# Performance work log

Measured on AMD Instinct MI355X. Metric: run time of the kernel, lower is better.

Reference implementation:

```python
import jax, jax.numpy as jnp
import numpy as np

N_NODES = 50000
N_EDGES = 800000


def _sage_conv(x, src, dst, Wl, Wr, b):
    # PyG SAGEConv (aggr='mean', root_weight=True):
    #   out_i = lin_l(mean_{j->i} x_j) + lin_r(x_i)
    msg = x[src]                                             # [E, F] gather
    agg = jax.ops.segment_sum(msg, dst, num_segments=N_NODES)
    deg = jax.ops.segment_sum(jnp.ones((msg.shape[0],), x.dtype), dst,
                              num_segments=N_NODES)
    agg = agg / jnp.maximum(deg, 1.0)[:, None]               # mean aggregation
    return agg @ Wl + x @ Wr + b


def setup_inputs() -> dict:
    key = jax.random.key(0)
    ks = jax.random.split(key, 9)
    Fin, H1, H2, Fout = 128, 256, 128, 64

    def w(k, fi, fo):
        return jax.random.normal(k, (fi, fo), jnp.float32) / np.sqrt(fi)

    return {
        "x": jax.random.normal(ks[0], (N_NODES, Fin), jnp.float32),
        "edge_index": jax.random.randint(ks[1], (2, N_EDGES), 0, N_NODES,
                                         dtype=jnp.int64),
        "Wl1": w(ks[2], Fin, H1), "Wr1": w(ks[3], Fin, H1),
        "b1": jnp.zeros((H1,), jnp.float32),
        "Wl2": w(ks[4], H1, H2), "Wr2": w(ks[5], H1, H2),
        "b2": jnp.zeros((H2,), jnp.float32),
        "Wl3": w(ks[6], H2, Fout), "Wr3": w(ks[7], H2, Fout),
        "b3": jnp.zeros((Fout,), jnp.float32),
    }


def reference(x, edge_index, Wl1, Wr1, b1, Wl2, Wr2, b2, Wl3, Wr3, b3):
    src, dst = edge_index[0], edge_index[1]
    # conv1 -> ReLU -> (dropout: identity in eval) -> conv2 -> ReLU -> conv3 -> Sigmoid
    h = jax.nn.relu(_sage_conv(x, src, dst, Wl1, Wr1, b1))
    h = jax.nn.relu(_sage_conv(h, src, dst, Wl2, Wr2, b2))
    out = jax.nn.sigmoid(_sage_conv(h, src, dst, Wl3, Wr3, b3))
    return out
```

## Files before the change

kernel.cpp:

```cpp
#include <hip/hip_runtime.h>
#include <cstddef>


using frag  = __attribute__((ext_vector_type(8))) short;
using f32x4 = __attribute__((ext_vector_type(4))) float;
using vf2   = __attribute__((ext_vector_type(2))) float;
typedef unsigned char u8;

constexpr int PBITS = 9;
constexpr int PSZ   = 1 << PBITS;
constexpr int PMAX  = 128;

__device__ __forceinline__ ushort f2bf(float f) {
    union { float f; unsigned u; } v; v.f = f;
    unsigned r = v.u + 0x7FFF + ((v.u >> 16) & 1);
    return (ushort)(r >> 16);
}
__device__ __forceinline__ float bf2f(ushort u) {
    union { unsigned u; float f; } v; v.u = ((unsigned)u) << 16;
    return v.f;
}


__global__ __launch_bounds__(256)
void k_pcount(const int* __restrict__ dst, int* __restrict__ pcount, int E, int P) {
    __shared__ int h[PMAX];
    int t = threadIdx.x;
    if (t < P) h[t] = 0;
    __syncthreads();
    int base = blockIdx.x * 4096;
    int n = min(4096, E - base);
    for (int i = t; i < n; i += 256)
        atomicAdd(&h[dst[base + i] >> PBITS], 1);
    __syncthreads();
    if (t < P && h[t]) atomicAdd(&pcount[t], h[t]);
}

__global__ void k_pscan(const int* __restrict__ pcount, int* __restrict__ pbase,
                        int* __restrict__ pcursor, int P) {
    if (threadIdx.x == 0) {
        int run = 0;
        for (int p = 0; p < P; ++p) { pbase[p] = run; pcursor[p] = run; run += pcount[p]; }
        pbase[P] = run;
    }
}

__global__ __launch_bounds__(256)
void k_scatter(const int* __restrict__ src, const int* __restrict__ dst,
               int* __restrict__ pcursor, unsigned* __restrict__ pairs, int E, int P) {
    __shared__ int h[PMAX];
    __shared__ int off[PMAX];
    int t = threadIdx.x;
    if (t < P) h[t] = 0;
    __syncthreads();
    int base = blockIdx.x * 4096;
    int pp[16]; int pr[16]; unsigned pk[16];
    #pragma unroll
    for (int ii = 0; ii < 16; ++ii) {
        int idx = base + ii * 256 + t;
        bool v = idx < E;
        int d = v ? dst[idx] : 0;
        int p = d >> PBITS;
        pp[ii] = v ? p : -1;
        pr[ii] = v ? atomicAdd(&h[p], 1) : 0;
        pk[ii] = v ? ((unsigned)src[idx] | ((unsigned)(d & (PSZ - 1)) << 16)) : 0u;
    }
    __syncthreads();
    if (t < P && h[t]) off[t] = atomicAdd(&pcursor[t], h[t]);
    __syncthreads();
    #pragma unroll
    for (int ii = 0; ii < 16; ++ii)
        if (pp[ii] >= 0) pairs[off[pp[ii]] + pr[ii]] = pk[ii];
}

__global__ __launch_bounds__(256)
void k_build(const unsigned* __restrict__ pairs, const int* __restrict__ pbase,
             int* __restrict__ deg, int* __restrict__ row_start,
             ushort* __restrict__ csr16, int M) {
    __shared__ int cnt[PSZ];
    __shared__ int ls[PSZ];
    __shared__ int fil[PSZ];
    __shared__ int ws[256];
    int pid = blockIdx.x;
    int t = threadIdx.x;
    int n0 = pid << PBITS;
    int L = min(PSZ, M - n0);
    int wb = pbase[pid], we = pbase[pid + 1];
    int ne = we - wb;
    for (int j = t; j < PSZ; j += 256) { cnt[j] = 0; fil[j] = 0; }
    __syncthreads();
    for (int i = t; i < ne; i += 256)
        atomicAdd(&cnt[pairs[wb + i] >> 16], 1);
    __syncthreads();
    int a = cnt[2 * t], b = cnt[2 * t + 1];
    ws[t] = a + b;
    __syncthreads();
    for (int o = 1; o < 256; o <<= 1) {
        int v = (t >= o) ? ws[t - o] : 0;
        __syncthreads();
        ws[t] += v;
        __syncthreads();
    }
    int excl = (t > 0) ? ws[t - 1] : 0;
    ls[2 * t] = excl; ls[2 * t + 1] = excl + a;
    __syncthreads();
    for (int j = t; j < L; j += 256) {
        deg[n0 + j] = cnt[j];
        row_start[n0 + j] = wb + ls[j];
    }
    for (int i = t; i < ne; i += 256) {
        unsigned pk = pairs[wb + i];
        int ln = pk >> 16;
        int pos = wb + ls[ln] + atomicAdd(&fil[ln], 1);
        csr16[pos] = (ushort)(pk & 0xFFFFu);
    }
}


struct CvtDesc {
    const float* s[6];
    ushort*      d[6];
    int K[6];
    int N[6];
    int KD[6];
    int KO[6];
};

__global__ void k_cvt_all(CvtDesc c, const float* __restrict__ x,
                          ushort* __restrict__ AX, u8* __restrict__ x8,
                          int n4, int xblocks) {
    int bid = blockIdx.x;
    if (bid < xblocks) {
        int i = bid * 256 + threadIdx.x;
        if (i < n4) {
            int row = i >> 5;
            int c4  = i & 31;
            float4 v = ((const float4*)x)[i];
            ushort4 o; o.x = f2bf(v.x); o.y = f2bf(v.y); o.z = f2bf(v.z); o.w = f2bf(v.w);
            *(ushort4*)(AX + (size_t)row * 256 + 128 + c4 * 4) = o;
            int pk = __builtin_amdgcn_cvt_pk_fp8_f32(v.x, v.y, 0, false);
            pk = __builtin_amdgcn_cvt_pk_fp8_f32(v.z, v.w, pk, true);
            *(int*)(x8 + (size_t)row * 128 + c4 * 4) = pk;
        }
    } else {
        int wb = bid - xblocks;
        int wi = wb >> 7;
        int t = (wb & 127) * 256 + threadIdx.x;
        int K = c.K[wi], N = c.N[wi];
        if (t < K * N) {
            int k = t / N, n = t % N;
            c.d[wi][(size_t)n * c.KD[wi] + c.KO[wi] + k] = f2bf(c.s[wi][t]);
        }
    }
}


template <int F, int EPI, int IN8, int LDI, int LDO>
__global__ __launch_bounds__(256)
void agg_bf(const void* __restrict__ inv, const ushort* __restrict__ csr16,
            const int* __restrict__ row_start, const int* __restrict__ deg,
            const ushort* __restrict__ u, const float* __restrict__ bias,
            void* __restrict__ out, int nN) {
    constexpr int GPL = F / 4;
    constexpr int NPB = 256 / GPL;
    int gid  = threadIdx.x / GPL;
    int li   = threadIdx.x % GPL;
    int node = blockIdx.x * NPB + gid;
    bool valid = node < nN;
    int start = valid ? row_start[node] : 0;
    int d     = valid ? deg[node] : 0;
    float a0 = 0.f, a1 = 0.f, a2 = 0.f, a3 = 0.f;

    auto gat = [&](int j) {
        int s = csr16[start + j];
        if constexpr (IN8) {
            int uu = *(const int*)((const u8*)inv + (size_t)s * LDI + li * 4);
            vf2 lo = __builtin_amdgcn_cvt_pk_f32_fp8(uu, false);
            vf2 hi = __builtin_amdgcn_cvt_pk_f32_fp8(uu, true);
            a0 += lo[0]; a1 += lo[1]; a2 += hi[0]; a3 += hi[1];
        } else {
            ushort4 uv = *(const ushort4*)((const ushort*)inv + (size_t)s * LDI + li * 4);
            a0 += bf2f(uv.x); a1 += bf2f(uv.y); a2 += bf2f(uv.z); a3 += bf2f(uv.w);
        }
    };

    int j = 0;
    for (; j + 8 <= d; j += 8) {
        gat(j); gat(j+1); gat(j+2); gat(j+3);
        gat(j+4); gat(j+5); gat(j+6); gat(j+7);
    }
    for (; j + 2 <= d; j += 2) { gat(j); gat(j+1); }
    for (; j < d; ++j) gat(j);

    if (!valid) return;
    float inv_d = 1.f / (float)(d > 0 ? d : 1);
    a0 *= inv_d; a1 *= inv_d; a2 *= inv_d; a3 *= inv_d;

    size_t o4 = (size_t)node * LDO + li * 4;
    if constexpr (EPI == 0) {
        ushort4 o; o.x = f2bf(a0); o.y = f2bf(a1); o.z = f2bf(a2); o.w = f2bf(a3);
        *(ushort4*)((ushort*)out + o4) = o;
    } else {
        ushort4 uv = *(const ushort4*)(u + (size_t)node * F + li * 4);
        float4 bv = *(const float4*)(bias + li * 4);
        a0 += bf2f(uv.x) + bv.x;
        a1 += bf2f(uv.y) + bv.y;
        a2 += bf2f(uv.z) + bv.z;
        a3 += bf2f(uv.w) + bv.w;
        if constexpr (EPI == 1) {
            ushort4 o;
            o.x = f2bf(fmaxf(a0, 0.f)); o.y = f2bf(fmaxf(a1, 0.f));
            o.z = f2bf(fmaxf(a2, 0.f)); o.w = f2bf(fmaxf(a3, 0.f));
            *(ushort4*)((ushort*)out + o4) = o;
        } else {
            float4 o;
            o.x = 1.f / (1.f + __expf(-a0)); o.y = 1.f / (1.f + __expf(-a1));
            o.z = 1.f / (1.f + __expf(-a2)); o.w = 1.f / (1.f + __expf(-a3));
            *(float4*)((float*)out + o4) = o;
        }
    }
}


__device__ __forceinline__ void gload16(const ushort* gp, char* lp) {
    __builtin_amdgcn_global_load_lds(
        (const __attribute__((address_space(1))) void*)gp,
        (__attribute__((address_space(3))) void*)lp, 16, 0, 0);
}

template <int BM, int BN, int K, int ACT, int OUT8>
__global__ __launch_bounds__(256)
void mgemm(const ushort* __restrict__ A, const ushort* __restrict__ B,
           const float* __restrict__ bias,
           void* __restrict__ C1, int ld1,
           ushort* __restrict__ C2, int ld2, int nsplit,
           int M, int N) {
    constexpr int NW = 4;
    constexpr int WM = 2, WN = 2;
    constexpr int MF = BM / (WM * 16);
    constexpr int NF = BN / (WN * 16);
    constexpr int NSTEP = K / 64;
    constexpr int TB = (BM + BN) * 128;
    __shared__ char lds[2 * TB];

    const int tid  = threadIdx.x;
    const int lane = tid & 63;
    const int wid  = tid >> 6;
    const int wm   = wid % WM, wn = wid / WM;
    const int bm   = blockIdx.x * BM;
    const int bn   = blockIdx.y * BN;
    const int l15  = lane & 15;
    const int lhi  = lane >> 4;
    const int lr8  = lane >> 3;
    const int lf   = lane & 7;

    auto stage = [&](int buf, int k0) {
        char* As = lds + buf * TB;
        char* Bs = As + BM * 128;
        #pragma unroll
        for (int it = 0; it < BM / (8 * NW); ++it) {
            int r0 = (it * NW + wid) * 8;
            int row = r0 + lr8;
            int gr = bm + row; if (gr >= M) gr = M - 1;
            int gfc = lf ^ (row & 7);
            gload16(A + (size_t)gr * K + k0 + gfc * 8, As + r0 * 128);
        }
        #pragma unroll
        for (int it = 0; it < BN / (8 * NW); ++it) {
            int r0 = (it * NW + wid) * 8;
            int row = r0 + lr8;
            int gfc = lf ^ (row & 7);
            gload16(B + (size_t)(bn + row) * K + k0 + gfc * 8, Bs + r0 * 128);
        }
    };

    f32x4 acc[MF][NF] = {};

    stage(0, 0);
    #pragma unroll
    for (int s = 0; s < NSTEP; ++s) {
        __syncthreads();
        if (s + 1 < NSTEP) stage((s + 1) & 1, (s + 1) * 64);
        char* As = lds + (s & 1) * TB;
        char* Bs = As + BM * 128;
        #pragma unroll
        for (int ks = 0; ks < 2; ++ks) {
            const int kb = ks * 64 + lhi * 16;
            frag a[MF], b[NF];
            #pragma unroll
            for (int mf = 0; mf < MF; ++mf) {
                int row = wm * MF * 16 + mf * 16 + l15;
                a[mf] = *(const frag*)(As + row * 128 + (kb ^ ((row & 7) << 4)));
            }
            #pragma unroll
            for (int nf = 0; nf < NF; ++nf) {
                int row = wn * NF * 16 + nf * 16 + l15;
                b[nf] = *(const frag*)(Bs + row * 128 + (kb ^ ((row & 7) << 4)));
            }
            #pragma unroll
            for (int mf = 0; mf < MF; ++mf)
                #pragma unroll
                for (int nf = 0; nf < NF; ++nf)
                    acc[mf][nf] = __builtin_amdgcn_mfma_f32_16x16x32_bf16(
                        a[mf], b[nf], acc[mf][nf], 0, 0, 0);
        }
    }

    #pragma unroll
    for (int mf = 0; mf < MF; ++mf) {
        #pragma unroll
        for (int r = 0; r < 4; ++r) {
            int gm = bm + wm * MF * 16 + mf * 16 + lhi * 4 + r;
            if (gm >= M) continue;
            #pragma unroll
            for (int nf = 0; nf < NF; ++nf) {
                int gn = bn + wn * NF * 16 + nf * 16 + l15;
                float v = acc[mf][nf][r];
                if (bias) v += bias[gn];
                if (ACT == 1) v = fmaxf(v, 0.f);
                if (gn < nsplit) {
                    if constexpr (OUT8) {
                        int pk = __builtin_amdgcn_cvt_pk_fp8_f32(v, v, 0, false);
                        ((u8*)C1)[(size_t)gm * ld1 + gn] = (u8)(pk & 0xFF);
                    } else {
                        ((ushort*)C1)[(size_t)gm * ld1 + gn] = f2bf(v);
                    }
                } else {
                    C2[(size_t)gm * ld2 + (gn - nsplit)] = f2bf(v);
                }
            }
        }
    }
}


extern "C" void kernel_launch(void* const* d_in, const int* in_sizes, int n_in,
                              void* d_out, int out_size, void* d_ws, size_t ws_size,
                              hipStream_t stream) {
    const float* x   = (const float*)d_in[0];
    const int*   ei  = (const int*)d_in[1];
    const float* Wl1 = (const float*)d_in[2];
    const float* Wr1 = (const float*)d_in[3];
    const float* b1  = (const float*)d_in[4];
    const float* Wl2 = (const float*)d_in[5];
    const float* Wr2 = (const float*)d_in[6];
    const float* b2  = (const float*)d_in[7];
    const float* Wl3 = (const float*)d_in[8];
    const float* Wr3 = (const float*)d_in[9];
    const float* b3  = (const float*)d_in[10];

    const int M = in_sizes[0] / 128;
    const int E = in_sizes[1] / 2;
    const int P = (M + PSZ - 1) / PSZ;
    const int* src = ei;
    const int* dst = ei + E;

    char* w = (char*)d_ws;
    auto alloc = [&](size_t bytes) -> void* {
        void* p = (void*)w;
        w += (bytes + 255) & ~(size_t)255;
        return p;
    };
    int* pcount    = (int*)alloc((size_t)PMAX * 4);
    int* pbase     = (int*)alloc((size_t)(PMAX + 1) * 4);
    int* pcursor   = (int*)alloc((size_t)PMAX * 4);
    unsigned* pairs = (unsigned*)alloc((size_t)E * 4);
    ushort* csr16  = (ushort*)alloc((size_t)E * 2);
    int* deg       = (int*)alloc((size_t)M * 4);
    int* row_start = (int*)alloc((size_t)M * 4);
    ushort* Wcat1T = (ushort*)alloc(256 * 256 * 2);
    ushort* Wcat2T = (ushort*)alloc(256 * 256 * 2);
    ushort* Wcat3T = (ushort*)alloc(128 * 128 * 2);
    ushort* AX   = (ushort*)alloc((size_t)M * 256 * 2);
    ushort* bufB = (ushort*)alloc((size_t)M * 128 * 2);
    ushort* bufH = (ushort*)alloc((size_t)M * 256 * 2);
    ushort* bufC = (ushort*)alloc((size_t)M * 128 * 2);
    u8* fp8buf   = (u8*)alloc((size_t)M * 128);
    (void)ws_size; (void)n_in; (void)out_size;

    ushort* h2 = bufB;
    ushort* h1 = bufH;
    ushort* u2 = bufC;   ushort* u3 = bufC;
    u8* x8   = fp8buf;   u8* t2_8 = fp8buf;   u8* t3_8 = fp8buf;

    hipMemsetAsync(pcount, 0, (size_t)PMAX * 4, stream);
    const int nchunk = (E + 4095) / 4096;
    k_pcount<<<nchunk, 256, 0, stream>>>(dst, pcount, E, P);
    k_pscan<<<1, 64, 0, stream>>>(pcount, pbase, pcursor, P);
    k_scatter<<<nchunk, 256, 0, stream>>>(src, dst, pcursor, pairs, E, P);
    k_build<<<P, 256, 0, stream>>>(pairs, pbase, deg, row_start, csr16, M);

    CvtDesc cd;
    cd.s[0] = Wl1; cd.d[0] = Wcat1T;           cd.K[0] = 128; cd.N[0] = 256; cd.KD[0] = 256; cd.KO[0] = 0;
    cd.s[1] = Wr1; cd.d[1] = Wcat1T;           cd.K[1] = 128; cd.N[1] = 256; cd.KD[1] = 256; cd.KO[1] = 128;
    cd.s[2] = Wl2; cd.d[2] = Wcat2T;           cd.K[2] = 256; cd.N[2] = 128; cd.KD[2] = 256; cd.KO[2] = 0;
    cd.s[3] = Wr2; cd.d[3] = Wcat2T + 128*256; cd.K[3] = 256; cd.N[3] = 128; cd.KD[3] = 256; cd.KO[3] = 0;
    cd.s[4] = Wl3; cd.d[4] = Wcat3T;           cd.K[4] = 128; cd.N[4] = 64;  cd.KD[4] = 128; cd.KO[4] = 0;
    cd.s[5] = Wr3; cd.d[5] = Wcat3T + 64*128;  cd.K[5] = 128; cd.N[5] = 64;  cd.KD[5] = 128; cd.KO[5] = 0;
    const int n4 = M * 128 / 4;
    const int xblocks = (n4 + 255) / 256;
    k_cvt_all<<<xblocks + 6 * 128, 256, 0, stream>>>(cd, x, AX, x8, n4, xblocks);

    const int gm64 = (M + 63) / 64;
    const int ga128 = (M + 7) / 8;
    const int ga64  = (M + 15) / 16;

    agg_bf<128, 0, 1, 128, 256><<<ga128, 256, 0, stream>>>(
        x8, csr16, row_start, deg, nullptr, nullptr, AX, M);
    mgemm<64, 64, 256, 1, 0><<<dim3(gm64, 4), 256, 0, stream>>>(
        AX, Wcat1T, b1, h1, 256, h1, 256, 256, M, 256);

    mgemm<64, 64, 256, 0, 1><<<dim3(gm64, 4), 256, 0, stream>>>(
        h1, Wcat2T, nullptr, t2_8, 128, u2, 128, 128, M, 256);
    agg_bf<128, 1, 1, 128, 128><<<ga128, 256, 0, stream>>>(
        t2_8, csr16, row_start, deg, u2, b2, h2, M);

    mgemm<64, 64, 128, 0, 1><<<dim3(gm64, 2), 256, 0, stream>>>(
        h2, Wcat3T, nullptr, t3_8, 64, u3, 64, 64, M, 128);
    agg_bf<64, 2, 1, 64, 64><<<ga64, 256, 0, stream>>>(
        t3_8, csr16, row_start, deg, u3, b3, (float*)d_out, M);
}
```

Measured before the change: 189.3 us.

## Fuse graph-build and conversion kernels into one cooperative persistent kernel

Replaces the memset plus the partition-count, scan, scatter, CSR-build and weight/feature conversion launches with a single cooperative kernel of 512 blocks. Phases are separated by grid-wide syncs. Conversion work units are spread over the blocks left idle in each graph-build phase, so the conversion overlaps the graph work. This removes several launch gaps and the separate conversion pass, at the cost of four grid barriers and a cooperative-launch requirement.

After: 426.8 us. 2.25x slower.

```diff
diff --git a/kernel.cpp b/kernel.cpp
--- a/kernel.cpp
+++ b/kernel.cpp
@@ -1,5 +1,8 @@
 #include <hip/hip_runtime.h>
+#include <hip/hip_cooperative_groups.h>
 #include <cstddef>
+
+namespace cg = cooperative_groups;
 
 
 using frag  = __attribute__((ext_vector_type(8))) short;
@@ -19,101 +22,6 @@
 __device__ __forceinline__ float bf2f(ushort u) {
     union { unsigned u; float f; } v; v.u = ((unsigned)u) << 16;
     return v.f;
-}
-
-
-__global__ __launch_bounds__(256)
-void k_pcount(const int* __restrict__ dst, int* __restrict__ pcount, int E, int P) {
-    __shared__ int h[PMAX];
-    int t = threadIdx.x;
-    if (t < P) h[t] = 0;
-    __syncthreads();
-    int base = blockIdx.x * 4096;
-    int n = min(4096, E - base);
-    for (int i = t; i < n; i += 256)
-        atomicAdd(&h[dst[base + i] >> PBITS], 1);
-    __syncthreads();
-    if (t < P && h[t]) atomicAdd(&pcount[t], h[t]);
-}
-
-__global__ void k_pscan(const int* __restrict__ pcount, int* __restrict__ pbase,
-                        int* __restrict__ pcursor, int P) {
-    if (threadIdx.x == 0) {
-        int run = 0;
-        for (int p = 0; p < P; ++p) { pbase[p] = run; pcursor[p] = run; run += pcount[p]; }
-        pbase[P] = run;
-    }
-}
-
-__global__ __launch_bounds__(256)
-void k_scatter(const int* __restrict__ src, const int* __restrict__ dst,
-               int* __restrict__ pcursor, unsigned* __restrict__ pairs, int E, int P) {
-    __shared__ int h[PMAX];
-    __shared__ int off[PMAX];
-    int t = threadIdx.x;
-    if (t < P) h[t] = 0;
-    __syncthreads();
-    int base = blockIdx.x * 4096;
-    int pp[16]; int pr[16]; unsigned pk[16];
-    #pragma unroll
-    for (int ii = 0; ii < 16; ++ii) {
-        int idx = base + ii * 256 + t;
-        bool v = idx < E;
-        int d = v ? dst[idx] : 0;
-        int p = d >> PBITS;
-        pp[ii] = v ? p : -1;
-        pr[ii] = v ? atomicAdd(&h[p], 1) : 0;
-        pk[ii] = v ? ((unsigned)src[idx] | ((unsigned)(d & (PSZ - 1)) << 16)) : 0u;
-    }
-    __syncthreads();
-    if (t < P && h[t]) off[t] = atomicAdd(&pcursor[t], h[t]);
-    __syncthreads();
-    #pragma unroll
-    for (int ii = 0; ii < 16; ++ii)
-        if (pp[ii] >= 0) pairs[off[pp[ii]] + pr[ii]] = pk[ii];
-}
-
-__global__ __launch_bounds__(256)
-void k_build(const unsigned* __restrict__ pairs, const int* __restrict__ pbase,
-             int* __restrict__ deg, int* __restrict__ row_start,
-             ushort* __restrict__ csr16, int M) {
-    __shared__ int cnt[PSZ];
-    __shared__ int ls[PSZ];
-    __shared__ int fil[PSZ];
-    __shared__ int ws[256];
-    int pid = blockIdx.x;
-    int t = threadIdx.x;
-    int n0 = pid << PBITS;
-    int L = min(PSZ, M - n0);
-    int wb = pbase[pid], we = pbase[pid + 1];
-    int ne = we - wb;
-    for (int j = t; j < PSZ; j += 256) { cnt[j] = 0; fil[j] = 0; }
-    __syncthreads();
-    for (int i = t; i < ne; i += 256)
-        atomicAdd(&cnt[pairs[wb + i] >> 16], 1);
-    __syncthreads();
-    int a = cnt[2 * t], b = cnt[2 * t + 1];
-    ws[t] = a + b;
-    __syncthreads();
-    for (int o = 1; o < 256; o <<= 1) {
-        int v = (t >= o) ? ws[t - o] : 0;
-        __syncthreads();
-        ws[t] += v;
-        __syncthreads();
-    }
-    int excl = (t > 0) ? ws[t - 1] : 0;
-    ls[2 * t] = excl; ls[2 * t + 1] = excl + a;
-    __syncthreads();
-    for (int j = t; j < L; j += 256) {
-        deg[n0 + j] = cnt[j];
-        row_start[n0 + j] = wb + ls[j];
-    }
-    for (int i = t; i < ne; i += 256) {
-        unsigned pk = pairs[wb + i];
-        int ln = pk >> 16;
-        int pos = wb + ls[ln] + atomicAdd(&fil[ln], 1);
-        csr16[pos] = (ushort)(pk & 0xFFFFu);
-    }
 }
 
 
@@ -126,12 +34,14 @@
     int KO[6];
 };
 
-__global__ void k_cvt_all(CvtDesc c, const float* __restrict__ x,
-                          ushort* __restrict__ AX, u8* __restrict__ x8,
-                          int n4, int xblocks) {
-    int bid = blockIdx.x;
-    if (bid < xblocks) {
-        int i = bid * 256 + threadIdx.x;
+__device__ __forceinline__ void do_cvt_unit(int u, const CvtDesc& c,
+                                            const float* __restrict__ x,
+                                            ushort* __restrict__ AX,
+                                            u8* __restrict__ x8,
+                                            int n4, int xunits) {
+    int t = threadIdx.x;
+    if (u < xunits) {
+        int i = u * 256 + t;
         if (i < n4) {
             int row = i >> 5;
             int c4  = i & 31;
@@ -143,13 +53,142 @@
             *(int*)(x8 + (size_t)row * 128 + c4 * 4) = pk;
         }
     } else {
-        int wb = bid - xblocks;
+        int wb = u - xunits;
         int wi = wb >> 7;
-        int t = (wb & 127) * 256 + threadIdx.x;
+        int tt = (wb & 127) * 256 + t;
         int K = c.K[wi], N = c.N[wi];
-        if (t < K * N) {
-            int k = t / N, n = t % N;
-            c.d[wi][(size_t)n * c.KD[wi] + c.KO[wi] + k] = f2bf(c.s[wi][t]);
+        if (tt < K * N) {
+            int k = tt / N, n = tt % N;
+            c.d[wi][(size_t)n * c.KD[wi] + c.KO[wi] + k] = f2bf(c.s[wi][tt]);
+        }
+    }
+}
+
+
+__global__ __launch_bounds__(256)
+void k_prep(const float* __restrict__ x, const int* __restrict__ src,
+            const int* __restrict__ dst,
+            int* __restrict__ pcount, int* __restrict__ pbase,
+            int* __restrict__ pcursor, unsigned* __restrict__ pairs,
+            ushort* __restrict__ csr16, int* __restrict__ deg,
+            int* __restrict__ row_start,
+            CvtDesc cd, ushort* __restrict__ AX, u8* __restrict__ x8,
+            int M, int E, int P, int nchunk, int n4, int xunits, int tunits) {
+    cg::grid_group grid = cg::this_grid();
+    __shared__ int shA[PSZ];
+    __shared__ int shB[PSZ];
+    __shared__ int shC[PSZ];
+    __shared__ int shD[256];
+    const int b = blockIdx.x;
+    const int t = threadIdx.x;
+    const int NB = gridDim.x;
+
+    if (b == 0) {
+        if (t < PMAX) pcount[t] = 0;
+    } else {
+        int base = (b - 1) * 4;
+        #pragma unroll
+        for (int q = 0; q < 4; ++q) {
+            int u = base + q;
+            if (u < tunits) do_cvt_unit(u, cd, x, AX, x8, n4, xunits);
+        }
+    }
+    grid.sync();
+
+    const int ph1base = (NB - 1) * 4;
+    if (b < nchunk) {
+        if (t < P) shA[t] = 0;
+        __syncthreads();
+        int base = b * 4096;
+        int n = min(4096, E - base);
+        for (int i = t; i < n; i += 256)
+            atomicAdd(&shA[dst[base + i] >> PBITS], 1);
+        __syncthreads();
+        if (t < P && shA[t]) atomicAdd(&pcount[t], shA[t]);
+    } else {
+        int base = ph1base + (b - nchunk) * 6;
+        #pragma unroll
+        for (int q = 0; q < 6; ++q) {
+            int u = base + q;
+            if (u < tunits) do_cvt_unit(u, cd, x, AX, x8, n4, xunits);
+        }
+    }
+    grid.sync();
+
+    const int ph2base = ph1base + (NB - nchunk) * 6;
+    if (b == 0) {
+        if (t == 0) {
+            int run = 0;
+            for (int p = 0; p < P; ++p) {
+                pbase[p] = run; pcursor[p] = run; run += pcount[p];
+            }
+            pbase[P] = run;
+        }
+    } else {
+        int base = ph2base + (b - 1) * 7;
+        #pragma unroll
+        for (int q = 0; q < 7; ++q) {
+            int u = base + q;
+            if (u < tunits) do_cvt_unit(u, cd, x, AX, x8, n4, xunits);
+        }
+    }
+    grid.sync();
+
+    if (b < nchunk) {
+        if (t < P) shA[t] = 0;
+        __syncthreads();
+        int base = b * 4096;
+        int pp[16]; int pr[16]; unsigned pk[16];
+        #pragma unroll
+        for (int ii = 0; ii < 16; ++ii) {
+            int idx = base + ii * 256 + t;
+            bool v = idx < E;
+            int d = v ? dst[idx] : 0;
+            int p = d >> PBITS;
+            pp[ii] = v ? p : -1;
+            pr[ii] = v ? atomicAdd(&shA[p], 1) : 0;
+            pk[ii] = v ? ((unsigned)src[idx] | ((unsigned)(d & (PSZ - 1)) << 16)) : 0u;
+        }
+        __syncthreads();
+        if (t < P && shA[t]) shB[t] = atomicAdd(&pcursor[t], shA[t]);
+        __syncthreads();
+        #pragma unroll
+        for (int ii = 0; ii < 16; ++ii)
+            if (pp[ii] >= 0) pairs[shB[pp[ii]] + pr[ii]] = pk[ii];
+    }
+    grid.sync();
+
+    if (b < P) {
+        int n0 = b << PBITS;
+        int L = min(PSZ, M - n0);
+        int wb = pbase[b], we = pbase[b + 1];
+        int ne = we - wb;
+        for (int j = t; j < PSZ; j += 256) { shA[j] = 0; shC[j] = 0; }
+        __syncthreads();
+        for (int i = t; i < ne; i += 256)
+            atomicAdd(&shA[pairs[wb + i] >> 16], 1);
+        __syncthreads();
+        int a = shA[2 * t], bb = shA[2 * t + 1];
+        shD[t] = a + bb;
+        __syncthreads();
+        for (int o = 1; o < 256; o <<= 1) {
+            int v = (t >= o) ? shD[t - o] : 0;
+            __syncthreads();
+            shD[t] += v;
+            __syncthreads();
+        }
+        int excl = (t > 0) ? shD[t - 1] : 0;
+        shB[2 * t] = excl; shB[2 * t + 1] = excl + a;
+        __syncthreads();
+        for (int j = t; j < L; j += 256) {
+            deg[n0 + j] = shA[j];
+            row_start[n0 + j] = wb + shB[j];
+        }
+        for (int i = t; i < ne; i += 256) {
+            unsigned pk = pairs[wb + i];
+            int ln = pk >> 16;
+            int pos = wb + shB[ln] + atomicAdd(&shC[ln], 1);
+            csr16[pos] = (ushort)(pk & 0xFFFFu);
         }
     }
 }
@@ -383,13 +422,6 @@
     ushort* u2 = bufC;   ushort* u3 = bufC;
     u8* x8   = fp8buf;   u8* t2_8 = fp8buf;   u8* t3_8 = fp8buf;
 
-    hipMemsetAsync(pcount, 0, (size_t)PMAX * 4, stream);
-    const int nchunk = (E + 4095) / 4096;
-    k_pcount<<<nchunk, 256, 0, stream>>>(dst, pcount, E, P);
-    k_pscan<<<1, 64, 0, stream>>>(pcount, pbase, pcursor, P);
-    k_scatter<<<nchunk, 256, 0, stream>>>(src, dst, pcursor, pairs, E, P);
-    k_build<<<P, 256, 0, stream>>>(pairs, pbase, deg, row_start, csr16, M);
-
     CvtDesc cd;
     cd.s[0] = Wl1; cd.d[0] = Wcat1T;           cd.K[0] = 128; cd.N[0] = 256; cd.KD[0] = 256; cd.KO[0] = 0;
     cd.s[1] = Wr1; cd.d[1] = Wcat1T;           cd.K[1] = 128; cd.N[1] = 256; cd.KD[1] = 256; cd.KO[1] = 128;
@@ -397,9 +429,24 @@
     cd.s[3] = Wr2; cd.d[3] = Wcat2T + 128*256; cd.K[3] = 256; cd.N[3] = 128; cd.KD[3] = 256; cd.KO[3] = 0;
     cd.s[4] = Wl3; cd.d[4] = Wcat3T;           cd.K[4] = 128; cd.N[4] = 64;  cd.KD[4] = 128; cd.KO[4] = 0;
     cd.s[5] = Wr3; cd.d[5] = Wcat3T + 64*128;  cd.K[5] = 128; cd.N[5] = 64;  cd.KD[5] = 128; cd.KO[5] = 0;
-    const int n4 = M * 128 / 4;
-    const int xblocks = (n4 + 255) / 256;
-    k_cvt_all<<<xblocks + 6 * 128, 256, 0, stream>>>(cd, x, AX, x8, n4, xblocks);
+
+    int nchunk = (E + 4095) / 4096;
+    int n4 = M * 128 / 4;
+    int xunits = (n4 + 255) / 256;
+    int tunits = xunits + 6 * 128;
+
+    {
+        const float* xa = x; const int* sa = src; const int* da = dst;
+        int Ma = M, Ea = E, Pa = P;
+        void* args[] = { (void*)&xa, (void*)&sa, (void*)&da,
+                         (void*)&pcount, (void*)&pbase, (void*)&pcursor,
+                         (void*)&pairs, (void*)&csr16, (void*)&deg,
+                         (void*)&row_start, (void*)&cd, (void*)&AX, (void*)&x8,
+                         (void*)&Ma, (void*)&Ea, (void*)&Pa, (void*)&nchunk,
+                         (void*)&n4, (void*)&xunits, (void*)&tunits };
+        hipLaunchCooperativeKernel((void*)k_prep, dim3(512), dim3(256),
+                                   args, 0, stream);
+    }
 
     const int gm64 = (M + 63) / 64;
     const int ga128 = (M + 7) / 8;
```
